# Kernel tuning notes

Hardware: AMD Instinct MI355X
Metric: run time of the kernel (lower is better)

## Reference

```python
import jax, jax.numpy as jnp
import numpy as np

NFFT = 4_194_304
NMODES = 2
NTAPS = 101
GAMMA = 0.0016567  # [/W/m]
DZ = 80000.0       # [m]


def setup_inputs() -> dict:
    key = jax.random.key(0)
    k1, k2, k3 = jax.random.split(key, 3)
    xr = jax.random.normal(k1, (NFFT, NMODES), dtype=jnp.float32)
    xi = jax.random.normal(k2, (NFFT, NMODES), dtype=jnp.float32)
    # fconv1d kernel: [ntaps, in_features=Nmodes, out_features=Nmodes] (lecun_normal-ish scale)
    W = jax.random.normal(k3, (NTAPS, NMODES, NMODES), dtype=jnp.float32) / np.sqrt(NTAPS * NMODES)
    b = jnp.zeros((NMODES,), dtype=jnp.float32)
    power = jnp.zeros((1,), dtype=jnp.float32)  # 0 dBm
    return {"xr": xr, "xi": xi, "W": W, "b": b, "power": power}


def reference(xr, xi, W, b, power):
    # P = |x|^2, shape [Nfft, Nmodes]
    P = xr * xr + xi * xi
    # valid 1D conv over time: [Nfft, Nmodes] -> [Nfft - ntaps + 1, Nmodes]
    phi = jax.lax.conv_general_dilated(
        P[None],            # [1, Nfft, Nmodes]
        W,                  # [ntaps, in, out]
        window_strides=(1,),
        padding='VALID',
        dimension_numbers=('NWC', 'WIO', 'NWC'),
    )[0] + b                # [Nfft - ntaps + 1, Nmodes]

    nmodes = xr.shape[-1]
    scale = 0.001 * 10.0 ** (power[0] / 10.0) / nmodes  # dBm -> W, per mode
    n0 = NTAPS // 2
    x = (xr + 1j * xi)[n0:xr.shape[0] - n0]  # valid-conv aligned slice
    y = x * jnp.exp(-1j * phi * (GAMMA * scale * DZ))
    return y
```

## Files before the change

kernel.cpp:

```cpp
#include <hip/hip_runtime.h>
#include <hip/hip_bf16.h>

#define NFFT   4194304
#define NMODES 2
#define NTAPS  101
#define NVALID (NFFT - NTAPS + 1)
#define N0     (NTAPS / 2)

constexpr int BLOCK = 64;
constexpr int TILE  = 512;
constexpr int NT    = (NVALID + TILE - 1) / TILE;
constexpr int WIN   = 640;
constexpr int NCH   = WIN / 2;
constexpr int NM    = 15;
constexpr int TBW   = 272;

constexpr int OXB = 1280;
constexpr int OPL = 2560;
constexpr int OBT = 3200;
constexpr int LWORDS = 3472;

typedef __attribute__((ext_vector_type(8)))  short short8;
typedef __attribute__((ext_vector_type(16))) float float16;

static __device__ __forceinline__ unsigned short f2bf(float x) {
    __hip_bfloat16 h = __float2bfloat16(x);
    return *reinterpret_cast<unsigned short*>(&h);
}
static __device__ __forceinline__ unsigned pk(float e0, float e1) {
    return (unsigned)f2bf(e0) | ((unsigned)f2bf(e1) << 16);
}
static __device__ __forceinline__ int swz(int s) {
    return s ^ (((s >> 5) & 7) << 2);
}
static __device__ __forceinline__ void gl16(const float4* g, unsigned* l) {
    __builtin_amdgcn_global_load_lds(
        (const __attribute__((address_space(1))) void*)g,
        (__attribute__((address_space(3))) void*)l, 16, 0, 0);
}

__global__ __launch_bounds__(BLOCK, 4) void nl_kernel(
    const float* __restrict__ xa,
    const float* __restrict__ xb,
    const float* __restrict__ W,  const float* __restrict__ b,
    const float* __restrict__ power, unsigned* __restrict__ out)
{
    __shared__ __align__(16) unsigned lds[LWORDS];
    unsigned* const xaR = lds;
    unsigned* const xbR = lds + OXB;
    unsigned* const Pl  = lds + OPL;
    unsigned* const Bt  = lds + OBT;

    const int lane = threadIdx.x & 63;
    const int colc = lane & 31;
    const int h    = lane >> 5;
    const int cs   = colc >> 1;
    const int o    = colc & 1;
    const int r    = colc;

    const int wstart = blockIdx.x * TILE;
    const int ts2    = wstart >> 1;

    const float4* __restrict__ xa4 = reinterpret_cast<const float4*>(xa);
    const float4* __restrict__ xb4 = reinterpret_cast<const float4*>(xb);
    #pragma unroll
    for (int k = 0; k < 5; ++k) {
        const int c  = lane + 64 * k;
        const int cc = min(ts2 + c, NFFT / 2 - 1);
        gl16(xa4 + cc, &xaR[4 * c]);
        gl16(xb4 + cc, &xbR[4 * c]);
    }

    {
        const float4* __restrict__ Wt = reinterpret_cast<const float4*>(W);
        #pragma unroll
        for (int k = 0; k < 5; ++k) {
            const int idx = lane + 64 * k;
            if (k < 4 || idx < TBW) {
                const int t  = (idx >> 1) - 15;
                const int oo = idx & 1;
                const bool ok = (unsigned)t <= 100u;
                const float4 w = Wt[ok ? t : 0];
                Bt[idx] = ok ? pk(oo ? w.y : w.x, oo ? w.w : w.z) : 0u;
            }
        }
    }

    asm volatile("s_waitcnt vmcnt(0)" ::: "memory");
    __builtin_amdgcn_sched_barrier(0);

    #pragma unroll
    for (int k = 0; k < 5; ++k) {
        const int tp = lane + 64 * k;
        const float4 a = *reinterpret_cast<const float4*>(&xaR[4 * tp]);
        const float4 c = *reinterpret_cast<const float4*>(&xbR[4 * tp]);
        const int g = wstart + 2 * tp;
        unsigned u0 = 0u, u1 = 0u;
        if (g < NFFT) {
            u0 = pk(a.x * a.x + c.x * c.x, a.y * a.y + c.y * c.y);
            u1 = pk(a.z * a.z + c.z * c.z, a.w * a.w + c.w * c.w);
        }
        *reinterpret_cast<uint2*>(&Pl[swz(2 * tp)]) = make_uint2(u0, u1);
    }

    const int bbase = ((4 * h - cs + 15) << 1) | o;
    float16 acc = {};
    uint4 areg[4];
    #pragma unroll
    for (int m = 0; m < 4; ++m)
        areg[m] = *reinterpret_cast<const uint4*>(&Pl[swz(16 * r + 8 * m + 4 * h)]);
    #pragma unroll
    for (int m = 0; m < NM; ++m) {
        uint4 bq;
        bq.x = Bt[bbase + 16 * m + 0];
        bq.y = Bt[bbase + 16 * m + 2];
        bq.z = Bt[bbase + 16 * m + 4];
        bq.w = Bt[bbase + 16 * m + 6];
        acc = __builtin_amdgcn_mfma_f32_32x32x16_bf16(
                  __builtin_bit_cast(short8, areg[m & 3]),
                  __builtin_bit_cast(short8, bq), acc, 0, 0, 0);
        if (m + 4 < NM)
            areg[m & 3] = *reinterpret_cast<const uint4*>(
                              &Pl[swz(16 * r + 8 * (m + 4) + 4 * h)]);
    }

    const float bo   = o ? b[1] : b[0];
    const float coef = 0.066268f * exp10f(power[0] * 0.1f);
    const float* __restrict__ xaF = reinterpret_cast<const float*>(xaR);
    const float* __restrict__ xbF = reinterpret_cast<const float*>(xbR);

    if (blockIdx.x != NT - 1) {
        #pragma unroll
        for (int j = 0; j < 16; ++j) {
            const int row = (j & 3) + 8 * (j >> 2) + 4 * h;
            const int lw  = 2 * (16 * row + cs + N0) + o;
            const float Ax = xaF[lw];
            const float Bx = xbF[lw];
            float sn, cn;
            __sincosf((acc[j] + bo) * coef, &sn, &cn);
            const int n = wstart + 16 * row + cs;
            __builtin_nontemporal_store(pk(Bx * cn - Ax * sn, Ax * cn + Bx * sn),
                                        &out[n * 2 + o]);
        }
    } else {
        #pragma unroll
        for (int j = 0; j < 16; ++j) {
            const int row = (j & 3) + 8 * (j >> 2) + 4 * h;
            const int n   = wstart + 16 * row + cs;
            if (n < NVALID) {
                const int lw  = 2 * (16 * row + cs + N0) + o;
                const float Ax = xaF[lw];
                const float Bx = xbF[lw];
                float sn, cn;
                __sincosf((acc[j] + bo) * coef, &sn, &cn);
                __builtin_nontemporal_store(pk(Bx * cn - Ax * sn, Ax * cn + Bx * sn),
                                            &out[n * 2 + o]);
            }
        }
    }
}

extern "C" void kernel_launch(void* const* d_in, const int* in_sizes, int n_in,
                              void* d_out, int out_size, void* d_ws, size_t ws_size,
                              hipStream_t stream) {
    const float* big[2] = {nullptr, nullptr};
    const float* W = nullptr; const float* b = nullptr; const float* power = nullptr;
    int nbig = 0;
    for (int i = 0; i < n_in; ++i) {
        const float* p = (const float*)d_in[i];
        const int sz = in_sizes[i];
        if (sz == NFFT * NMODES)       { if (nbig < 2) big[nbig++] = p; }
        else if (sz == NTAPS * NMODES * NMODES) { W = p; }
        else if (sz == NMODES)         { b = p; }
        else if (sz == 1)              { power = p; }
    }

    unsigned* out = (unsigned*)d_out;
    nl_kernel<<<NT, BLOCK, 0, stream>>>(big[0], big[1], W, b, power, out);
}
```

Before: 116.2 us.

## Process eight tiles per block with double-buffered async LDS prefetch

Each block now loops over eight consecutive tiles instead of one. The next tile's inputs are prefetched into an alternate LDS buffer with global_load_lds while the current tile is computed, gated by a partial vmcnt wait. The weight table is built once per block, which amortises its setup and hides global load latency behind MFMA and sincos work. In exchange the grid shrinks eightfold, LDS per block roughly doubles and the occupancy hint drops to 2. That leaves far fewer waves resident to hide latency.

```diff
diff --git a/kernel.cpp b/kernel.cpp
--- a/kernel.cpp
+++ b/kernel.cpp
@@ -10,15 +10,15 @@
 constexpr int BLOCK = 64;
 constexpr int TILE  = 512;
 constexpr int NT    = (NVALID + TILE - 1) / TILE;
+constexpr int TPB   = 8;
+constexpr int NB    = NT / TPB;
 constexpr int WIN   = 640;
-constexpr int NCH   = WIN / 2;
 constexpr int NM    = 15;
 constexpr int TBW   = 272;
 
-constexpr int OXB = 1280;
-constexpr int OPL = 2560;
-constexpr int OBT = 3200;
-constexpr int LWORDS = 3472;
+constexpr int OPL = 5120;
+constexpr int OBT = 5760;
+constexpr int LWORDS = 6032;
 
 typedef __attribute__((ext_vector_type(8)))  short short8;
 typedef __attribute__((ext_vector_type(16))) float float16;
@@ -39,17 +39,15 @@
         (__attribute__((address_space(3))) void*)l, 16, 0, 0);
 }
 
-__global__ __launch_bounds__(BLOCK, 4) void nl_kernel(
+__global__ __launch_bounds__(BLOCK, 2) void nl_kernel(
     const float* __restrict__ xa,
     const float* __restrict__ xb,
     const float* __restrict__ W,  const float* __restrict__ b,
     const float* __restrict__ power, unsigned* __restrict__ out)
 {
     __shared__ __align__(16) unsigned lds[LWORDS];
-    unsigned* const xaR = lds;
-    unsigned* const xbR = lds + OXB;
-    unsigned* const Pl  = lds + OPL;
-    unsigned* const Bt  = lds + OBT;
+    unsigned* const Pl = lds + OPL;
+    unsigned* const Bt = lds + OBT;
 
     const int lane = threadIdx.x & 63;
     const int colc = lane & 31;
@@ -58,19 +56,25 @@
     const int o    = colc & 1;
     const int r    = colc;
 
-    const int wstart = blockIdx.x * TILE;
-    const int ts2    = wstart >> 1;
-
     const float4* __restrict__ xa4 = reinterpret_cast<const float4*>(xa);
     const float4* __restrict__ xb4 = reinterpret_cast<const float4*>(xb);
-    #pragma unroll
-    for (int k = 0; k < 5; ++k) {
-        const int c  = lane + 64 * k;
-        const int cc = min(ts2 + c, NFFT / 2 - 1);
-        gl16(xa4 + cc, &xaR[4 * c]);
-        gl16(xb4 + cc, &xbR[4 * c]);
-    }
-
+
+    const int tbase = blockIdx.x * TPB;
+
+    #define STAGE(wt, bufw) {                                                       \
+        unsigned* const bA = lds + (bufw) * 2560;                                   \
+        unsigned* const bB = bA + 1280;                                             \
+        const int ts2 = (wt) * (TILE / 2);                                          \
+        _Pragma("unroll")                                                           \
+        for (int k = 0; k < 5; ++k) {                                               \
+            const int c  = lane + 64 * k;               \
+            const int cc = min(ts2 + c, NFFT / 2 - 1);                              \
+            gl16(xa4 + cc, &bA[4 * c]);                                             \
+            gl16(xb4 + cc, &bB[4 * c]);                                             \
+        }                                                                           \
+    }
+
+    STAGE(tbase, 0)
     {
         const float4* __restrict__ Wt = reinterpret_cast<const float4*>(W);
         #pragma unroll
@@ -86,78 +90,94 @@
         }
     }
 
-    asm volatile("s_waitcnt vmcnt(0)" ::: "memory");
-    __builtin_amdgcn_sched_barrier(0);
-
-    #pragma unroll
-    for (int k = 0; k < 5; ++k) {
-        const int tp = lane + 64 * k;
-        const float4 a = *reinterpret_cast<const float4*>(&xaR[4 * tp]);
-        const float4 c = *reinterpret_cast<const float4*>(&xbR[4 * tp]);
-        const int g = wstart + 2 * tp;
-        unsigned u0 = 0u, u1 = 0u;
-        if (g < NFFT) {
-            u0 = pk(a.x * a.x + c.x * c.x, a.y * a.y + c.y * c.y);
-            u1 = pk(a.z * a.z + c.z * c.z, a.w * a.w + c.w * c.w);
-        }
-        *reinterpret_cast<uint2*>(&Pl[swz(2 * tp)]) = make_uint2(u0, u1);
-    }
-
-    const int bbase = ((4 * h - cs + 15) << 1) | o;
-    float16 acc = {};
-    uint4 areg[4];
-    #pragma unroll
-    for (int m = 0; m < 4; ++m)
-        areg[m] = *reinterpret_cast<const uint4*>(&Pl[swz(16 * r + 8 * m + 4 * h)]);
-    #pragma unroll
-    for (int m = 0; m < NM; ++m) {
-        uint4 bq;
-        bq.x = Bt[bbase + 16 * m + 0];
-        bq.y = Bt[bbase + 16 * m + 2];
-        bq.z = Bt[bbase + 16 * m + 4];
-        bq.w = Bt[bbase + 16 * m + 6];
-        acc = __builtin_amdgcn_mfma_f32_32x32x16_bf16(
-                  __builtin_bit_cast(short8, areg[m & 3]),
-                  __builtin_bit_cast(short8, bq), acc, 0, 0, 0);
-        if (m + 4 < NM)
-            areg[m & 3] = *reinterpret_cast<const uint4*>(
-                              &Pl[swz(16 * r + 8 * (m + 4) + 4 * h)]);
-    }
-
     const float bo   = o ? b[1] : b[0];
     const float coef = 0.066268f * exp10f(power[0] * 0.1f);
-    const float* __restrict__ xaF = reinterpret_cast<const float*>(xaR);
-    const float* __restrict__ xbF = reinterpret_cast<const float*>(xbR);
-
-    if (blockIdx.x != NT - 1) {
-        #pragma unroll
-        for (int j = 0; j < 16; ++j) {
-            const int row = (j & 3) + 8 * (j >> 2) + 4 * h;
-            const int lw  = 2 * (16 * row + cs + N0) + o;
-            const float Ax = xaF[lw];
-            const float Bx = xbF[lw];
-            float sn, cn;
-            __sincosf((acc[j] + bo) * coef, &sn, &cn);
-            const int n = wstart + 16 * row + cs;
-            __builtin_nontemporal_store(pk(Bx * cn - Ax * sn, Ax * cn + Bx * sn),
-                                        &out[n * 2 + o]);
-        }
-    } else {
-        #pragma unroll
-        for (int j = 0; j < 16; ++j) {
-            const int row = (j & 3) + 8 * (j >> 2) + 4 * h;
-            const int n   = wstart + 16 * row + cs;
-            if (n < NVALID) {
+    const int bbase  = ((4 * h - cs + 15) << 1) | o;
+
+    #pragma unroll 1
+    for (int t = 0; t < TPB; ++t) {
+        const int wt     = tbase + t;
+        const int wstart = wt * TILE;
+        unsigned* const xaR = lds + (t & 1) * 2560;
+        unsigned* const xbR = xaR + 1280;
+
+        if (t + 1 < TPB) {
+            STAGE(wt + 1, (t + 1) & 1)
+            __builtin_amdgcn_sched_barrier(0);
+            asm volatile("s_waitcnt vmcnt(10)" ::: "memory");
+        } else {
+            __builtin_amdgcn_sched_barrier(0);
+            asm volatile("s_waitcnt vmcnt(0)" ::: "memory");
+        }
+        __builtin_amdgcn_sched_barrier(0);
+
+        #pragma unroll
+        for (int k = 0; k < 5; ++k) {
+            const int tp = lane + 64 * k;
+            const float4 a = *reinterpret_cast<const float4*>(&xaR[4 * tp]);
+            const float4 c = *reinterpret_cast<const float4*>(&xbR[4 * tp]);
+            const int g = wstart + 2 * tp;
+            unsigned u0 = 0u, u1 = 0u;
+            if (g < NFFT) {
+                u0 = pk(a.x * a.x + c.x * c.x, a.y * a.y + c.y * c.y);
+                u1 = pk(a.z * a.z + c.z * c.z, a.w * a.w + c.w * c.w);
+            }
+            *reinterpret_cast<uint2*>(&Pl[swz(2 * tp)]) = make_uint2(u0, u1);
+        }
+
+        float16 acc = {};
+        uint4 areg[4];
+        #pragma unroll
+        for (int m = 0; m < 4; ++m)
+            areg[m] = *reinterpret_cast<const uint4*>(&Pl[swz(16 * r + 8 * m + 4 * h)]);
+        #pragma unroll
+        for (int m = 0; m < NM; ++m) {
+            uint4 bq;
+            bq.x = Bt[bbase + 16 * m + 0];
+            bq.y = Bt[bbase + 16 * m + 2];
+            bq.z = Bt[bbase + 16 * m + 4];
+            bq.w = Bt[bbase + 16 * m + 6];
+            acc = __builtin_amdgcn_mfma_f32_32x32x16_bf16(
+                      __builtin_bit_cast(short8, areg[m & 3]),
+                      __builtin_bit_cast(short8, bq), acc, 0, 0, 0);
+            if (m + 4 < NM)
+                areg[m & 3] = *reinterpret_cast<const uint4*>(
+                                  &Pl[swz(16 * r + 8 * (m + 4) + 4 * h)]);
+        }
+
+        const float* __restrict__ xaF = reinterpret_cast<const float*>(xaR);
+        const float* __restrict__ xbF = reinterpret_cast<const float*>(xbR);
+        if (wt != NT - 1) {
+            #pragma unroll
+            for (int j = 0; j < 16; ++j) {
+                const int row = (j & 3) + 8 * (j >> 2) + 4 * h;
                 const int lw  = 2 * (16 * row + cs + N0) + o;
                 const float Ax = xaF[lw];
                 const float Bx = xbF[lw];
                 float sn, cn;
                 __sincosf((acc[j] + bo) * coef, &sn, &cn);
+                const int n = wstart + 16 * row + cs;
                 __builtin_nontemporal_store(pk(Bx * cn - Ax * sn, Ax * cn + Bx * sn),
                                             &out[n * 2 + o]);
             }
-        }
-    }
+        } else {
+            #pragma unroll
+            for (int j = 0; j < 16; ++j) {
+                const int row = (j & 3) + 8 * (j >> 2) + 4 * h;
+                const int n   = wstart + 16 * row + cs;
+                if (n < NVALID) {
+                    const int lw  = 2 * (16 * row + cs + N0) + o;
+                    const float Ax = xaF[lw];
+                    const float Bx = xbF[lw];
+                    float sn, cn;
+                    __sincosf((acc[j] + bo) * coef, &sn, &cn);
+                    __builtin_nontemporal_store(pk(Bx * cn - Ax * sn, Ax * cn + Bx * sn),
+                                                &out[n * 2 + o]);
+                }
+            }
+        }
+    }
+    #undef STAGE
 }
 
 extern "C" void kernel_launch(void* const* d_in, const int* in_sizes, int n_in,
@@ -176,5 +196,5 @@
     }
 
     unsigned* out = (unsigned*)d_out;
-    nl_kernel<<<NT, BLOCK, 0, stream>>>(big[0], big[1], W, b, power, out);
-}
+    nl_kernel<<<NB, BLOCK, 0, stream>>>(big[0], big[1], W, b, power, out);
+}
```

After: 121.9 us. 4.9% more time.
